# Performance work log

Hardware: AMD Instinct MI355X
Metric: run time of the kernel (lower is better)

Reference implementation:

```python
import jax, jax.numpy as jnp
import numpy as np

DIM = 256
D_STATE = 16
D_INNER = 2 * DIM
D_CONV = 4
DT_RANK = (DIM + 15) // 16  # 'auto' = ceil(dim/16)
B_SZ, H, W = 8, 32, 32


def setup_inputs() -> dict:
    key = jax.random.key(0)
    ks = jax.random.split(key, 12)
    n = lambda k, s, sc=0.02: jax.random.normal(k, s, jnp.float32) * sc
    # Mamba1 dt init: dt ~ exp(U(log dt_min, log dt_max)), bias = inv_softplus(dt)
    dt = jnp.exp(jax.random.uniform(ks[5], (D_INNER,), jnp.float32,
                                    np.log(1e-3), np.log(1e-1)))
    return {
        "x": jax.random.normal(ks[0], (B_SZ, DIM, H, W), jnp.float32),
        "ln_g": jnp.ones((DIM,), jnp.float32),
        "ln_b": jnp.zeros((DIM,), jnp.float32),
        "in_proj_w": n(ks[1], (2 * D_INNER, DIM)),
        "conv_w": n(ks[2], (D_INNER, 1, D_CONV), 0.1),  # depthwise Conv1d kernel
        "conv_b": jnp.zeros((D_INNER,), jnp.float32),
        "x_proj_w": n(ks[3], (DT_RANK + 2 * D_STATE, D_INNER)),
        "dt_proj_w": n(ks[4], (D_INNER, DT_RANK), DT_RANK ** -0.5),
        "dt_proj_b": jnp.log(jnp.expm1(dt)),
        "A_log": jnp.log(jnp.broadcast_to(
            jnp.arange(1, D_STATE + 1, dtype=jnp.float32), (D_INNER, D_STATE))),
        "Dp": jnp.ones((D_INNER,), jnp.float32),
        "out_proj_w": n(ks[6], (DIM, D_INNER)),
        "mlp_ln_g": jnp.ones((DIM,), jnp.float32),
        "mlp_ln_b": jnp.zeros((DIM,), jnp.float32),
        "mlp_w1": n(ks[7], (4 * DIM, DIM)),
        "mlp_b1": jnp.zeros((4 * DIM,), jnp.float32),
        "mlp_w2": n(ks[8], (DIM, 4 * DIM)),
        "mlp_b2": jnp.zeros((DIM,), jnp.float32),
    }


def _layernorm(x, g, b):
    m = x.mean(-1, keepdims=True)
    v = x.var(-1, keepdims=True)
    return (x - m) * jax.lax.rsqrt(v + 1e-5) * g + b


def _selective_scan(u, dt, A, Bm, Cm, Dp):
    # u, dt: [B,L,Di]; Bm, Cm: [B,L,S]; A: [Di,S]; Dp: [Di]
    def step(h, t):
        dt_t, B_t, C_t, u_t = t  # [B,Di], [B,S], [B,S], [B,Di]
        dA = jnp.exp(dt_t[..., None] * A)                 # [B,Di,S]
        h = dA * h + dt_t[..., None] * B_t[:, None, :] * u_t[..., None]
        y = jnp.einsum('bds,bs->bd', h, C_t)
        return h, y

    h0 = jnp.zeros((u.shape[0], A.shape[0], A.shape[1]), u.dtype)
    xs = (dt.transpose(1, 0, 2), Bm.transpose(1, 0, 2),
          Cm.transpose(1, 0, 2), u.transpose(1, 0, 2))
    _, ys = jax.lax.scan(step, h0, xs)                    # ys: [L,B,Di]
    return ys.transpose(1, 0, 2) + u * Dp


def reference(x, ln_g, ln_b, in_proj_w, conv_w, conv_b, x_proj_w,
              dt_proj_w, dt_proj_b, A_log, Dp, out_proj_w,
              mlp_ln_g, mlp_ln_b, mlp_w1, mlp_b1, mlp_w2, mlp_b2):
    B, C, Hh, Ww = x.shape
    xf = x.reshape(B, C, Hh * Ww).transpose(0, 2, 1)      # [B,L,C]

    # ---- Mamba1 mixer with pre-LN residual ----
    xn = _layernorm(xf, ln_g, ln_b)
    xz = xn @ in_proj_w.T                                 # [B,L,2*Di]
    xi, z = jnp.split(xz, 2, axis=-1)
    # depthwise causal conv1d + SiLU
    xc = jax.lax.conv_general_dilated(
        xi.transpose(0, 2, 1), conv_w, (1,), [(D_CONV - 1, 0)],
        feature_group_count=D_INNER, dimension_numbers=('NCH', 'OIH', 'NCH'))
    xc = jax.nn.silu(xc + conv_b[None, :, None]).transpose(0, 2, 1)  # [B,L,Di]
    # input-dependent dt, B, C
    dbl = xc @ x_proj_w.T
    dt_r = dbl[..., :DT_RANK]
    Bm = dbl[..., DT_RANK:DT_RANK + D_STATE]
    Cm = dbl[..., DT_RANK + D_STATE:]
    dt = jax.nn.softplus(dt_r @ dt_proj_w.T + dt_proj_b)  # [B,L,Di]
    A = -jnp.exp(A_log)
    y = _selective_scan(xc, dt, A, Bm, Cm, Dp)
    y = y * jax.nn.silu(z)
    xf = xf + y @ out_proj_w.T

    # ---- gated MLP with pre-LN residual ----
    h = _layernorm(xf, mlp_ln_g, mlp_ln_b)
    h = jax.nn.gelu(h @ mlp_w1.T + mlp_b1, approximate=False) @ mlp_w2.T + mlp_b2
    xf = xf + h

    return xf.transpose(0, 2, 1).reshape(B, C, Hh, Ww)
```

## Files before the change

### kernel.cpp

```cpp
#include <hip/hip_runtime.h>
#include <math.h>

#define DIM      256
#define L_SEQ    1024
#define B_SZ     8
#define D_INNER  512
#define D_STATE  16
#define DT_RANK  16
#define N_TOK    (B_SZ * L_SEQ)

typedef unsigned short u16;
typedef __attribute__((ext_vector_type(4))) float f32x4;
typedef __attribute__((ext_vector_type(8))) short short8;
struct __align__(8) us4 { u16 x, y, z, w; };

#define OFF_XNB  0
#define OFF_XZ   1048576
#define OFF_XC   9437184
#define OFF_DBL  13631488
#define OFF_DT   14024704
#define OFF_XF2  18219008
#define OFF_YB   20316160
#define OFF_WB   22413312
#define WB_IN    0
#define WB_OUT   262144
#define WB_W1    393216
#define WB_W2    655360
#define WB_XP    917504

__device__ __forceinline__ u16 f2b(float f) {
    unsigned int u = __float_as_uint(f);
    return (u16)((u + 0x7fffu + ((u >> 16) & 1u)) >> 16);
}

__global__ __launch_bounds__(256) void cvt5_kernel(const float* __restrict__ a,
                                                   const float* __restrict__ b,
                                                   const float* __restrict__ c,
                                                   const float* __restrict__ d,
                                                   const float* __restrict__ e,
                                                   u16* __restrict__ out) {
    int i = blockIdx.x * 256 + threadIdx.x;
    const float* src; int off;
    if (i < 262144)      { src = a; off = i; }
    else if (i < 393216) { src = b; off = i - 262144; }
    else if (i < 655360) { src = c; off = i - 393216; }
    else if (i < 917504) { src = d; off = i - 655360; }
    else                 { src = e; off = i - 917504; }
    out[i] = f2b(src[off]);
}

__global__ __launch_bounds__(256) void ln_kernel(const float* __restrict__ in,
                                                 const float* __restrict__ g,
                                                 const float* __restrict__ b,
                                                 u16* __restrict__ out,
                                                 int transposed_in) {
    int token = blockIdx.x;
    int c = threadIdx.x;
    float v;
    if (transposed_in) {
        int bb = token >> 10, l = token & 1023;
        v = in[((size_t)bb * DIM + c) * L_SEQ + l];
    } else {
        v = in[(size_t)token * DIM + c];
    }
    float s = v, s2 = v * v;
    #pragma unroll
    for (int o = 32; o; o >>= 1) {
        s  += __shfl_down(s, o);
        s2 += __shfl_down(s2, o);
    }
    __shared__ float red[8];
    int w = threadIdx.x >> 6;
    if ((threadIdx.x & 63) == 0) { red[w] = s; red[4 + w] = s2; }
    __syncthreads();
    if (threadIdx.x == 0) {
        float a = 0.f, aa = 0.f;
        for (int i = 0; i < 4; i++) { a += red[i]; aa += red[4 + i]; }
        red[0] = a; red[4] = aa;
    }
    __syncthreads();
    float mean = red[0] * (1.f / DIM);
    float var  = red[4] * (1.f / DIM) - mean * mean;
    float rstd = rsqrtf(var + 1e-5f);
    out[(size_t)token * DIM + c] = f2b((v - mean) * rstd * g[c] + b[c]);
}

__device__ __forceinline__ void gload16(const void* g, void* l) {
    __builtin_amdgcn_global_load_lds(
        (const __attribute__((address_space(1))) unsigned int*)g,
        (__attribute__((address_space(3))) unsigned int*)l,
        16, 0, 0);
}

template <int EPI>
__global__ __launch_bounds__(256) void gemm_mfma(const u16* __restrict__ A,
                                                 const u16* __restrict__ W,
                                                 void* __restrict__ Cout,
                                                 int M, int N, int K,
                                                 const float* __restrict__ bias,
                                                 const float* __restrict__ extra) {
    __shared__ u16 Als[4096];
    __shared__ u16 Bls[4096];
    int tid = threadIdx.x;
    int w = tid >> 6, l = tid & 63;
    int m0 = blockIdx.y << 7, n0 = blockIdx.x << 7;

    int srow = tid >> 2;
    int scol = (tid & 3) << 3;
    const u16* Ag  = A + (size_t)(m0 + srow) * K + scol;
    const u16* Ag2 = A + (size_t)(m0 + 64 + srow) * K + scol;
    const u16* Wg  = W + (size_t)(n0 + srow) * K + scol;
    const u16* Wg2 = W + (size_t)(n0 + 64 + srow) * K + scol;
    u16* Ab0 = Als + (w << 9);
    u16* Ab1 = Als + 2048 + (w << 9);
    u16* Bb0 = Bls + (w << 9);
    u16* Bb1 = Bls + 2048 + (w << 9);

    int wr = (w >> 1) << 6, wc = (w & 1) << 6;
    int fr = l & 15, fk = (l >> 4) << 3;

    f32x4 acc[4][4] = {};
    for (int k0 = 0; k0 < K; k0 += 32) {
        gload16(Ag + k0, Ab0);
        gload16(Ag2 + k0, Ab1);
        gload16(Wg + k0, Bb0);
        gload16(Wg2 + k0, Bb1);
        __syncthreads();
        short8 af[4], bfr[4];
        #pragma unroll
        for (int i = 0; i < 4; i++)
            af[i] = *(const short8*)&Als[(wr + i * 16 + fr) * 32 + fk];
        #pragma unroll
        for (int j = 0; j < 4; j++)
            bfr[j] = *(const short8*)&Bls[(wc + j * 16 + fr) * 32 + fk];
        #pragma unroll
        for (int i = 0; i < 4; i++)
            #pragma unroll
            for (int j = 0; j < 4; j++)
                acc[i][j] = __builtin_amdgcn_mfma_f32_16x16x32_bf16(af[i], bfr[j], acc[i][j], 0, 0, 0);
        __syncthreads();
    }

    int cr = (l >> 4) << 2;
    int ccol = l & 15;
    #pragma unroll
    for (int i = 0; i < 4; i++) {
        #pragma unroll
        for (int j = 0; j < 4; j++) {
            int n = n0 + wc + j * 16 + ccol;
            #pragma unroll
            for (int r = 0; r < 4; r++) {
                int m = m0 + wr + i * 16 + cr + r;
                int bb = m >> 10, ll = m & 1023;
                float v = acc[i][j][r];
                if (EPI == 0) {
                    ((float*)Cout)[(size_t)m * N + n] = v;
                } else if (EPI == 1) {
                    ((float*)Cout)[(size_t)m * N + n] = v + extra[((size_t)bb * DIM + n) * L_SEQ + ll];
                } else if (EPI == 2) {
                    v += bias[n];
                    ((u16*)Cout)[(size_t)m * N + n] = f2b(0.5f * v * (1.f + erff(v * 0.70710678118f)));
                } else {
                    v += bias[n] + extra[(size_t)m * DIM + n];
                    ((float*)Cout)[((size_t)bb * DIM + n) * L_SEQ + ll] = v;
                }
            }
        }
    }
}

__global__ __launch_bounds__(256) void conv_kernel(const float* __restrict__ XZ,
                                                   const float* __restrict__ cw,
                                                   const float* __restrict__ cb,
                                                   float* __restrict__ XC,
                                                   u16* __restrict__ XCB) {
    int idx = blockIdx.x * 256 + threadIdx.x;
    int d = idx & 511;
    int token = idx >> 9;
    int l = token & 1023, b = token >> 10;
    const float* base = XZ + (size_t)b * L_SEQ * 1024 + d;
    float acc = cb[d];
    #pragma unroll
    for (int j = 0; j < 4; j++) {
        int ls = l - 3 + j;
        if (ls >= 0) acc = fmaf(base[(size_t)ls * 1024], cw[d * 4 + j], acc);
    }
    float v = acc / (1.f + __expf(-acc));
    XC[(size_t)token * 512 + d] = v;
    XCB[(size_t)token * 512 + d] = f2b(v);
}

__global__ __launch_bounds__(128) void xproj3_kernel(const u16* __restrict__ XCB,
                                                     const u16* __restrict__ WXP,
                                                     float* __restrict__ DBL) {
    __shared__ float dbl_s[32][49];
    int tid = threadIdx.x;
    int w = tid >> 6, l = tid & 63;
    int m0 = blockIdx.x << 5;
    int fr = l & 15, fk = (l >> 4) << 3;
    const u16* Ab = XCB + (size_t)(m0 + (w << 4) + fr) * 512 + fk;
    const u16* Wb = WXP + (size_t)fr * 512 + fk;
    f32x4 acc[3] = {};
    for (int k0 = 0; k0 < 512; k0 += 32) {
        short8 a0 = *(const short8*)(Ab + k0);
        short8 b0 = *(const short8*)(Wb + k0);
        short8 b1 = *(const short8*)(Wb + 16 * 512 + k0);
        short8 b2 = *(const short8*)(Wb + 32 * 512 + k0);
        acc[0] = __builtin_amdgcn_mfma_f32_16x16x32_bf16(a0, b0, acc[0], 0, 0, 0);
        acc[1] = __builtin_amdgcn_mfma_f32_16x16x32_bf16(a0, b1, acc[1], 0, 0, 0);
        acc[2] = __builtin_amdgcn_mfma_f32_16x16x32_bf16(a0, b2, acc[2], 0, 0, 0);
    }
    int cr = (l >> 4) << 2, ccol = l & 15;
    #pragma unroll
    for (int j = 0; j < 3; j++)
        #pragma unroll
        for (int r = 0; r < 4; r++)
            dbl_s[(w << 4) + cr + r][j * 16 + ccol] = acc[j][r];
    __syncthreads();
    #pragma unroll
    for (int it = 0; it < 3; it++) {
        int fidx = it * 512 + tid * 4;
        int row = fidx / 48, col = fidx % 48;
        float4 v;
        v.x = dbl_s[row][col]; v.y = dbl_s[row][col + 1];
        v.z = dbl_s[row][col + 2]; v.w = dbl_s[row][col + 3];
        *(float4*)(DBL + (size_t)(m0 + row) * 48 + col) = v;
    }
}

__global__ __launch_bounds__(256) void dtproj_kernel(const float* __restrict__ DBL,
                                                     const float* __restrict__ wdt,
                                                     const float* __restrict__ wdb,
                                                     float* __restrict__ DT) {
    int idx = blockIdx.x * 256 + threadIdx.x;
    int token = idx >> 7, q = idx & 127;
    int d0 = q << 2;
    const float4* dtr4 = (const float4*)(DBL + (size_t)token * 48);
    float4 t0 = dtr4[0], t1 = dtr4[1], t2 = dtr4[2], t3 = dtr4[3];
    float4 ov;
    #pragma unroll
    for (int qq = 0; qq < 4; qq++) {
        int d = d0 + qq;
        const float4* wr = (const float4*)(wdt + (size_t)d * 16);
        float4 w0 = wr[0], w1 = wr[1], w2 = wr[2], w3 = wr[3];
        float a = wdb[d];
        a += t0.x * w0.x + t0.y * w0.y + t0.z * w0.z + t0.w * w0.w;
        a += t1.x * w1.x + t1.y * w1.y + t1.z * w1.z + t1.w * w1.w;
        a += t2.x * w2.x + t2.y * w2.y + t2.z * w2.z + t2.w * w2.w;
        a += t3.x * w3.x + t3.y * w3.y + t3.z * w3.z + t3.w * w3.w;
        ((float*)&ov)[qq] = (a > 20.f) ? a : log1pf(__expf(a));
    }
    *(float4*)(DT + (size_t)token * 512 + d0) = ov;
}

#define T_CH 64
__global__ __launch_bounds__(256) void scan_kernel(const float* __restrict__ U,
                                                   const float* __restrict__ DBL,
                                                   const float* __restrict__ DT,
                                                   const float* __restrict__ XZ,
                                                   const float* __restrict__ A_log,
                                                   const float* __restrict__ Dp,
                                                   u16* __restrict__ YB) {
    __shared__ float s_dt[2][T_CH][16];
    __shared__ float s_u [2][T_CH][16];
    __shared__ float s_BC[2][T_CH][32];
    __shared__ float s_z [2][T_CH][16];
    __shared__ float s_y [2][T_CH * 17];

    int blk = blockIdx.x;
    int b = blk >> 5, ch = blk & 31;
    int tid = threadIdx.x;
    int s = tid & 15, dl = tid >> 4;
    int d = ch * 16 + dl;
    int w = tid >> 6;

    float Ads = -__expf(A_log[d * D_STATE + s]);
    float Dv = Dp[d];

    const float* DTb = DT  + (size_t)b * L_SEQ * D_INNER + ch * 16;
    const float* Ub  = U   + (size_t)b * L_SEQ * D_INNER + ch * 16;
    const float* DBb = DBL + (size_t)b * L_SEQ * 48 + 16;
    const float* Zb  = XZ  + (size_t)b * L_SEQ * 1024 + 512 + ch * 16;
    u16* Yb          = YB  + (size_t)b * L_SEQ * D_INNER + ch * 16;

    int r16 = tid >> 2, q16 = (tid & 3) << 2;
    int r32 = tid >> 3, q32 = (tid & 7) << 2;

    #define STAGE(c, bf) { \
        int t0_ = (c) * T_CH; \
        gload16(DTb + (size_t)(t0_ + r16) * 512 + q16, &s_dt[bf][0][0] + (w << 8)); \
        gload16(Ub  + (size_t)(t0_ + r16) * 512 + q16, &s_u [bf][0][0] + (w << 8)); \
        gload16(Zb  + (size_t)(t0_ + r16) * 1024 + q16, &s_z[bf][0][0] + (w << 8)); \
        gload16(DBb + (size_t)(t0_ + r32) * 48 + q32, &s_BC[bf][0][0] + (w << 8)); \
        gload16(DBb + (size_t)(t0_ + 32 + r32) * 48 + q32, &s_BC[bf][0][0] + 1024 + (w << 8)); \
    }

    float h = 0.f;
    int bf = 0;
    STAGE(0, 0);
    __syncthreads();

    for (int c = 0; c < L_SEQ / T_CH; c++) {
        if (c + 1 < L_SEQ / T_CH) STAGE(c + 1, bf ^ 1);
        int yb = c & 1;
        #pragma unroll 1
        for (int tb = 0; tb < 4; tb++) {
            float da[16], db[16], cc[16], pr[16];
            float myud = 0.f;
            #pragma unroll
            for (int j = 0; j < 16; j++) {
                int t = (tb << 4) + j;
                float dtv = s_dt[bf][t][dl];
                float uv  = s_u [bf][t][dl];
                float bs  = s_BC[bf][t][s];
                float cs  = s_BC[bf][t][16 + s];
                da[j] = __expf(dtv * Ads);
                db[j] = dtv * bs * uv;
                cc[j] = cs;
                myud = (s == j) ? uv * Dv : myud;
            }
            #pragma unroll
            for (int j = 0; j < 16; j++) {
                h = fmaf(da[j], h, db[j]);
                pr[j] = h * cc[j];
            }
            float w8[8];
            #pragma unroll
            for (int k = 0; k < 8; k++) {
                float a = pr[2 * k], bv = pr[2 * k + 1];
                float keep = (s & 1) ? bv : a;
                float send = (s & 1) ? a : bv;
                w8[k] = keep + __shfl_xor(send, 1);
            }
            float u4[4];
            #pragma unroll
            for (int k = 0; k < 4; k++) {
                float a = w8[2 * k], bv = w8[2 * k + 1];
                float keep = (s & 2) ? bv : a;
                float send = (s & 2) ? a : bv;
                u4[k] = keep + __shfl_xor(send, 2);
            }
            float x2[2];
            #pragma unroll
            for (int k = 0; k < 2; k++) {
                float a = u4[2 * k], bv = u4[2 * k + 1];
                float keep = (s & 4) ? bv : a;
                float send = (s & 4) ? a : bv;
                x2[k] = keep + __shfl_xor(send, 4);
            }
            float a0 = x2[0], b0 = x2[1];
            float keep = (s & 8) ? b0 : a0;
            float send = (s & 8) ? a0 : b0;
            float res = keep + __shfl_xor(send, 8);
            int t = (tb << 4) + s;
            float zv = s_z[bf][t][dl];
            float y = res + myud;
            s_y[yb][t * 17 + dl] = y * (zv / (1.f + __expf(-zv)));
        }
        __syncthreads();
        {
            int t0_ = c * T_CH;
            int tt = tid >> 2, qq = (tid & 3) << 2;
            us4 o;
            o.x = f2b(s_y[yb][tt * 17 + qq + 0]);
            o.y = f2b(s_y[yb][tt * 17 + qq + 1]);
            o.z = f2b(s_y[yb][tt * 17 + qq + 2]);
            o.w = f2b(s_y[yb][tt * 17 + qq + 3]);
            *(us4*)(Yb + (size_t)(t0_ + tt) * 512 + qq) = o;
        }
        bf ^= 1;
    }
    #undef STAGE
}

extern "C" void kernel_launch(void* const* d_in, const int* in_sizes, int n_in,
                              void* d_out, int out_size, void* d_ws, size_t ws_size,
                              hipStream_t stream) {
    (void)in_sizes; (void)n_in; (void)out_size; (void)ws_size;
    const float* x         = (const float*)d_in[0];
    const float* ln_g      = (const float*)d_in[1];
    const float* ln_b      = (const float*)d_in[2];
    const float* in_proj_w = (const float*)d_in[3];
    const float* conv_w    = (const float*)d_in[4];
    const float* conv_b    = (const float*)d_in[5];
    const float* x_proj_w  = (const float*)d_in[6];
    const float* dt_proj_w = (const float*)d_in[7];
    const float* dt_proj_b = (const float*)d_in[8];
    const float* A_log     = (const float*)d_in[9];
    const float* Dp        = (const float*)d_in[10];
    const float* out_proj_w= (const float*)d_in[11];
    const float* mlp_ln_g  = (const float*)d_in[12];
    const float* mlp_ln_b  = (const float*)d_in[13];
    const float* mlp_w1    = (const float*)d_in[14];
    const float* mlp_b1    = (const float*)d_in[15];
    const float* mlp_w2    = (const float*)d_in[16];
    const float* mlp_b2    = (const float*)d_in[17];

    float* ws  = (float*)d_ws;
    u16*   XNB = (u16*)(ws + OFF_XNB);
    u16*   XCB = (u16*)(ws + OFF_XNB);
    float* XZ  = ws + OFF_XZ;
    u16*   H   = (u16*)(ws + OFF_XZ);
    float* XC  = ws + OFF_XC;
    float* DBL = ws + OFF_DBL;
    float* DT  = ws + OFF_DT;
    float* XF2 = ws + OFF_XF2;
    u16*   YB  = (u16*)(ws + OFF_YB);
    u16*   WB  = (u16*)(ws + OFF_WB);
    float* out = (float*)d_out;

    cvt5_kernel<<<3680, 256, 0, stream>>>(in_proj_w, out_proj_w, mlp_w1, mlp_w2, x_proj_w, WB);
    ln_kernel<<<N_TOK, 256, 0, stream>>>(x, ln_g, ln_b, XNB, 1);
    gemm_mfma<0><<<dim3(8, 64), 256, 0, stream>>>(XNB, WB + WB_IN, XZ, N_TOK, 1024, 256, nullptr, nullptr);
    conv_kernel<<<(N_TOK * D_INNER) / 256, 256, 0, stream>>>(XZ, conv_w, conv_b, XC, XCB);
    xproj3_kernel<<<256, 128, 0, stream>>>(XCB, WB + WB_XP, DBL);
    dtproj_kernel<<<4096, 256, 0, stream>>>(DBL, dt_proj_w, dt_proj_b, DT);
    scan_kernel<<<256, 256, 0, stream>>>(XC, DBL, DT, XZ, A_log, Dp, YB);
    gemm_mfma<1><<<dim3(2, 64), 256, 0, stream>>>(YB, WB + WB_OUT, XF2, N_TOK, 256, 512, nullptr, x);
    ln_kernel<<<N_TOK, 256, 0, stream>>>(XF2, mlp_ln_g, mlp_ln_b, XNB, 0);
    gemm_mfma<2><<<dim3(8, 64), 256, 0, stream>>>(XNB, WB + WB_W1, H, N_TOK, 1024, 256, mlp_b1, nullptr);
    gemm_mfma<3><<<dim3(2, 64), 256, 0, stream>>>(H, WB + WB_W2, out, N_TOK, 256, 1024, mlp_b2, XF2);
}
```

Measured before the change: 332.0 us.

## Transpose input and output with tiled LDS kernels instead of strided accesses

Adds explicit LDS-tiled transpose kernels for the NCHW input and output. The first layernorm, the out-proj residual and the final GEMM epilogue now use contiguous token-major accesses instead of strided reads and writes. The bf16 copy of the conv output is also dropped, and xproj converts fp32 to bf16 on the fly, which saves a store but doubles its reads. The cost is two extra launches and a full extra read and write of the input and output tensors.

After: 324.3 us. -2.3%, faster.

```diff
diff --git a/kernel.cpp b/kernel.cpp
--- a/kernel.cpp
+++ b/kernel.cpp
@@ -8,20 +8,24 @@
 #define D_STATE  16
 #define DT_RANK  16
 #define N_TOK    (B_SZ * L_SEQ)
+#define T_CH     64
 
 typedef unsigned short u16;
 typedef __attribute__((ext_vector_type(4))) float f32x4;
 typedef __attribute__((ext_vector_type(8))) short short8;
 struct __align__(8) us4 { u16 x, y, z, w; };
 
-#define OFF_XNB  0
-#define OFF_XZ   1048576
-#define OFF_XC   9437184
-#define OFF_DBL  13631488
-#define OFF_DT   14024704
-#define OFF_XF2  18219008
-#define OFF_YB   20316160
-#define OFF_WB   22413312
+#define OFF_WB   0
+#define OFF_XT   471040
+#define OFF_XNB  2568192
+#define OFF_XZ   3616768
+#define OFF_XC   12005376
+#define OFF_DBL  16199680
+#define OFF_DT   16592896
+#define OFF_YB   20787200
+#define OFF_XF2  OFF_XC
+#define OFF_TOUT (OFF_XC + 2097152)
+#define OFF_H    OFF_XZ
 #define WB_IN    0
 #define WB_OUT   262144
 #define WB_W1    393216
@@ -49,20 +53,41 @@
     out[i] = f2b(src[off]);
 }
 
+__global__ __launch_bounds__(256) void tin_kernel(const float* __restrict__ x,
+                                                  float* __restrict__ XT) {
+    __shared__ float tile[64][65];
+    int bb = blockIdx.x >> 6, c0 = ((blockIdx.x >> 4) & 3) << 6, l0 = (blockIdx.x & 15) << 6;
+    int tr = threadIdx.x >> 6, tc = threadIdx.x & 63;
+    const float* src = x + ((size_t)bb * 256 + c0) * 1024 + l0;
+    #pragma unroll
+    for (int i = 0; i < 16; i++) tile[tr + i * 4][tc] = src[(size_t)(tr + i * 4) * 1024 + tc];
+    __syncthreads();
+    float* dst = XT + ((size_t)bb * 1024 + l0) * 256 + c0;
+    #pragma unroll
+    for (int i = 0; i < 16; i++) dst[(size_t)(tr + i * 4) * 256 + tc] = tile[tc][tr + i * 4];
+}
+
+__global__ __launch_bounds__(256) void tout_kernel(const float* __restrict__ T,
+                                                   float* __restrict__ outp) {
+    __shared__ float tile[64][65];
+    int bb = blockIdx.x >> 6, c0 = ((blockIdx.x >> 4) & 3) << 6, l0 = (blockIdx.x & 15) << 6;
+    int tr = threadIdx.x >> 6, tc = threadIdx.x & 63;
+    const float* src = T + ((size_t)bb * 1024 + l0) * 256 + c0;
+    #pragma unroll
+    for (int i = 0; i < 16; i++) tile[tr + i * 4][tc] = src[(size_t)(tr + i * 4) * 256 + tc];
+    __syncthreads();
+    float* dst = outp + ((size_t)bb * 256 + c0) * 1024 + l0;
+    #pragma unroll
+    for (int i = 0; i < 16; i++) dst[(size_t)(tr + i * 4) * 1024 + tc] = tile[tc][tr + i * 4];
+}
+
 __global__ __launch_bounds__(256) void ln_kernel(const float* __restrict__ in,
                                                  const float* __restrict__ g,
                                                  const float* __restrict__ b,
-                                                 u16* __restrict__ out,
-                                                 int transposed_in) {
+                                                 u16* __restrict__ out) {
     int token = blockIdx.x;
     int c = threadIdx.x;
-    float v;
-    if (transposed_in) {
-        int bb = token >> 10, l = token & 1023;
-        v = in[((size_t)bb * DIM + c) * L_SEQ + l];
-    } else {
-        v = in[(size_t)token * DIM + c];
-    }
+    float v = in[(size_t)token * DIM + c];
     float s = v, s2 = v * v;
     #pragma unroll
     for (int o = 32; o; o >>= 1) {
@@ -151,18 +176,17 @@
             #pragma unroll
             for (int r = 0; r < 4; r++) {
                 int m = m0 + wr + i * 16 + cr + r;
-                int bb = m >> 10, ll = m & 1023;
                 float v = acc[i][j][r];
                 if (EPI == 0) {
                     ((float*)Cout)[(size_t)m * N + n] = v;
                 } else if (EPI == 1) {
-                    ((float*)Cout)[(size_t)m * N + n] = v + extra[((size_t)bb * DIM + n) * L_SEQ + ll];
+                    ((float*)Cout)[(size_t)m * N + n] = v + extra[(size_t)m * DIM + n];
                 } else if (EPI == 2) {
                     v += bias[n];
                     ((u16*)Cout)[(size_t)m * N + n] = f2b(0.5f * v * (1.f + erff(v * 0.70710678118f)));
                 } else {
                     v += bias[n] + extra[(size_t)m * DIM + n];
-                    ((float*)Cout)[((size_t)bb * DIM + n) * L_SEQ + ll] = v;
+                    ((float*)Cout)[(size_t)m * N + n] = v;
                 }
             }
         }
@@ -172,8 +196,7 @@
 __global__ __launch_bounds__(256) void conv_kernel(const float* __restrict__ XZ,
                                                    const float* __restrict__ cw,
                                                    const float* __restrict__ cb,
-                                                   float* __restrict__ XC,
-                                                   u16* __restrict__ XCB) {
+                                                   float* __restrict__ XC) {
     int idx = blockIdx.x * 256 + threadIdx.x;
     int d = idx & 511;
     int token = idx >> 9;
@@ -185,12 +208,10 @@
         int ls = l - 3 + j;
         if (ls >= 0) acc = fmaf(base[(size_t)ls * 1024], cw[d * 4 + j], acc);
     }
-    float v = acc / (1.f + __expf(-acc));
-    XC[(size_t)token * 512 + d] = v;
-    XCB[(size_t)token * 512 + d] = f2b(v);
-}
-
-__global__ __launch_bounds__(128) void xproj3_kernel(const u16* __restrict__ XCB,
+    XC[(size_t)token * 512 + d] = acc / (1.f + __expf(-acc));
+}
+
+__global__ __launch_bounds__(128) void xproj3_kernel(const float* __restrict__ XCf,
                                                      const u16* __restrict__ WXP,
                                                      float* __restrict__ DBL) {
     __shared__ float dbl_s[32][49];
@@ -198,11 +219,17 @@
     int w = tid >> 6, l = tid & 63;
     int m0 = blockIdx.x << 5;
     int fr = l & 15, fk = (l >> 4) << 3;
-    const u16* Ab = XCB + (size_t)(m0 + (w << 4) + fr) * 512 + fk;
+    const float* Af = XCf + (size_t)(m0 + (w << 4) + fr) * 512 + fk;
     const u16* Wb = WXP + (size_t)fr * 512 + fk;
     f32x4 acc[3] = {};
     for (int k0 = 0; k0 < 512; k0 += 32) {
-        short8 a0 = *(const short8*)(Ab + k0);
+        float4 fa = *(const float4*)(Af + k0);
+        float4 fb = *(const float4*)(Af + k0 + 4);
+        short8 a0;
+        a0[0] = (short)f2b(fa.x); a0[1] = (short)f2b(fa.y);
+        a0[2] = (short)f2b(fa.z); a0[3] = (short)f2b(fa.w);
+        a0[4] = (short)f2b(fb.x); a0[5] = (short)f2b(fb.y);
+        a0[6] = (short)f2b(fb.z); a0[7] = (short)f2b(fb.w);
         short8 b0 = *(const short8*)(Wb + k0);
         short8 b1 = *(const short8*)(Wb + 16 * 512 + k0);
         short8 b2 = *(const short8*)(Wb + 32 * 512 + k0);
@@ -253,7 +280,6 @@
     *(float4*)(DT + (size_t)token * 512 + d0) = ov;
 }
 
-#define T_CH 64
 __global__ __launch_bounds__(256) void scan_kernel(const float* __restrict__ U,
                                                    const float* __restrict__ DBL,
                                                    const float* __restrict__ DT,
@@ -397,27 +423,30 @@
     const float* mlp_b2    = (const float*)d_in[17];
 
     float* ws  = (float*)d_ws;
+    u16*   WB  = (u16*)(ws + OFF_WB);
+    float* XT  = ws + OFF_XT;
     u16*   XNB = (u16*)(ws + OFF_XNB);
-    u16*   XCB = (u16*)(ws + OFF_XNB);
     float* XZ  = ws + OFF_XZ;
-    u16*   H   = (u16*)(ws + OFF_XZ);
     float* XC  = ws + OFF_XC;
     float* DBL = ws + OFF_DBL;
     float* DT  = ws + OFF_DT;
+    u16*   YB  = (u16*)(ws + OFF_YB);
     float* XF2 = ws + OFF_XF2;
-    u16*   YB  = (u16*)(ws + OFF_YB);
-    u16*   WB  = (u16*)(ws + OFF_WB);
+    float* TOUT= ws + OFF_TOUT;
+    u16*   H   = (u16*)(ws + OFF_H);
     float* out = (float*)d_out;
 
     cvt5_kernel<<<3680, 256, 0, stream>>>(in_proj_w, out_proj_w, mlp_w1, mlp_w2, x_proj_w, WB);
-    ln_kernel<<<N_TOK, 256, 0, stream>>>(x, ln_g, ln_b, XNB, 1);
+    tin_kernel<<<512, 256, 0, stream>>>(x, XT);
+    ln_kernel<<<N_TOK, 256, 0, stream>>>(XT, ln_g, ln_b, XNB);
     gemm_mfma<0><<<dim3(8, 64), 256, 0, stream>>>(XNB, WB + WB_IN, XZ, N_TOK, 1024, 256, nullptr, nullptr);
-    conv_kernel<<<(N_TOK * D_INNER) / 256, 256, 0, stream>>>(XZ, conv_w, conv_b, XC, XCB);
-    xproj3_kernel<<<256, 128, 0, stream>>>(XCB, WB + WB_XP, DBL);
+    conv_kernel<<<(N_TOK * D_INNER) / 256, 256, 0, stream>>>(XZ, conv_w, conv_b, XC);
+    xproj3_kernel<<<256, 128, 0, stream>>>(XC, WB + WB_XP, DBL);
     dtproj_kernel<<<4096, 256, 0, stream>>>(DBL, dt_proj_w, dt_proj_b, DT);
     scan_kernel<<<256, 256, 0, stream>>>(XC, DBL, DT, XZ, A_log, Dp, YB);
-    gemm_mfma<1><<<dim3(2, 64), 256, 0, stream>>>(YB, WB + WB_OUT, XF2, N_TOK, 256, 512, nullptr, x);
-    ln_kernel<<<N_TOK, 256, 0, stream>>>(XF2, mlp_ln_g, mlp_ln_b, XNB, 0);
+    gemm_mfma<1><<<dim3(2, 64), 256, 0, stream>>>(YB, WB + WB_OUT, XF2, N_TOK, 256, 512, nullptr, XT);
+    ln_kernel<<<N_TOK, 256, 0, stream>>>(XF2, mlp_ln_g, mlp_ln_b, XNB);
     gemm_mfma<2><<<dim3(8, 64), 256, 0, stream>>>(XNB, WB + WB_W1, H, N_TOK, 1024, 256, mlp_b1, nullptr);
-    gemm_mfma<3><<<dim3(2, 64), 256, 0, stream>>>(H, WB + WB_W2, out, N_TOK, 256, 1024, mlp_b2, XF2);
-}
+    gemm_mfma<3><<<dim3(2, 64), 256, 0, stream>>>(H, WB + WB_W2, TOUT, N_TOK, 256, 1024, mlp_b2, XF2);
+    tout_kernel<<<512, 256, 0, stream>>>(TOUT, out);
+}
```
